# Optimization experiments

Measured on AMD Instinct MI355X. Metric: run time of the kernel, lower is better.

Reference implementation:

```python
import jax, jax.numpy as jnp
import numpy as np

NUM_CLASSES = 10
HIDDEN = 64
_LABEL2MASK_THRESHOL = 500


def setup_inputs() -> dict:
    key = jax.random.key(0)
    ks = jax.random.split(key, 8)
    B, h, w = 4, 60, 80
    feature1 = jax.random.normal(ks[0], (B, 512, h, w), dtype=jnp.float32)
    feature2 = jax.random.normal(ks[1], (B, 512, h // 2, w // 2), dtype=jnp.float32)
    # kaiming fan_in init for 1x1 convs: std = sqrt(2/fan_in)
    w1 = jax.random.normal(ks[2], (HIDDEN, 512), dtype=jnp.float32) * np.sqrt(2.0 / 512)
    b1 = jnp.zeros((HIDDEN,), dtype=jnp.float32)
    w2 = jax.random.normal(ks[3], (HIDDEN, 512), dtype=jnp.float32) * np.sqrt(2.0 / 512)
    b2 = jnp.zeros((HIDDEN,), dtype=jnp.float32)
    wo = jax.random.normal(ks[4], (NUM_CLASSES + 1, HIDDEN), dtype=jnp.float32) * np.sqrt(2.0 / HIDDEN)
    bo = jnp.zeros((NUM_CLASSES + 1,), dtype=jnp.float32)
    return {"feature1": feature1, "feature2": feature2, "w1": w1, "b1": b1,
            "w2": w2, "b2": b2, "wo": wo, "bo": bo}


def conv1x1(x, w, b):
    # x: (B,C,H,W), w: (O,C) -> (B,O,H,W)
    return jnp.einsum('bchw,oc->bohw', x, w) + b[None, :, None, None]


def label2bbx(seg, num_classes):
    # seg: (B,H,W) int labels. Vectorized per-(batch,class) min/max reduction
    # replacing the original python double loop. Fixed output shape
    # (B*(num_classes-1), 6); rows failing the pixel-count threshold are -1.
    B, H, W = seg.shape
    classes = jnp.arange(1, num_classes)  # cls_id != 0, covers 1..num_classes-1
    mask = seg[:, None, :, :] == classes[None, :, None, None]  # (B,C-1,H,W)
    count = mask.sum(axis=(2, 3))
    xs = jnp.arange(W)
    ys = jnp.arange(H)
    big = jnp.int32(2 ** 30)
    xmin = jnp.where(mask, xs[None, None, None, :], big).min(axis=(2, 3))
    xmax = jnp.where(mask, xs[None, None, None, :], -1).max(axis=(2, 3))
    ymin = jnp.where(mask, ys[None, None, :, None], big).min(axis=(2, 3))
    ymax = jnp.where(mask, ys[None, None, :, None], -1).max(axis=(2, 3))
    valid = count >= _LABEL2MASK_THRESHOL
    batch_ids = jnp.broadcast_to(jnp.arange(B)[:, None], (B, num_classes - 1))
    cls_ids = jnp.broadcast_to(classes[None, :], (B, num_classes - 1))
    rows = jnp.stack([batch_ids, xmin, ymin, xmax, ymax, cls_ids], axis=-1)
    rows = jnp.where(valid[..., None], rows, -1)
    return rows.reshape(-1, 6)


def reference(feature1, feature2, w1, b1, w2, b2, wo, bo):
    feat1 = jax.nn.relu(conv1x1(feature1, w1, b1))          # (B,64,h,w)
    feat2 = jax.nn.relu(conv1x1(feature2, w2, b2))          # (B,64,h/2,w/2)
    feat2_up = jnp.repeat(jnp.repeat(feat2, 2, axis=2), 2, axis=3)
    combo = feat1 + feat2_up
    # nearest upsample scale_factor=8
    combo_up = jnp.repeat(jnp.repeat(combo, 8, axis=2), 8, axis=3)  # (B,64,8h,8w)
    out = jax.nn.relu(conv1x1(combo_up, wo, bo))            # (B,11,8h,8w)
    probability = jax.nn.softmax(out, axis=1)
    segmentation = jnp.argmax(probability, axis=1)
    bbx = label2bbx(segmentation, NUM_CLASSES)
    return probability, segmentation, bbx
```

## Files before the change

kernel.cpp:

```cpp
#include <hip/hip_runtime.h>
#include <math.h>

#define NB   4
#define CIN  512
#define HID  64
#define NK   11
#define H1   60
#define W1p  80
#define P1   4800
#define H2   30
#define W2p  40
#define P2   1200
#define HO   480
#define WOp  640
#define NP1  (NB*P1)
#define NP2  (NB*P2)
#define PLANE ((size_t)HO*WOp)
#define SEG_OFF ((size_t)NB*NK*PLANE)
#define BBX_OFF (SEG_OFF + (size_t)NB*PLANE)

#define WS_C1  65536
#define WS_F2  (WS_C1 + NP1*64)
#define WS_PRB (WS_F2 + NP2*64)
#define WS_SEG (WS_PRB + NP1*12)

typedef __attribute__((ext_vector_type(8))) short bf16x8;
typedef __attribute__((ext_vector_type(4))) float f32x4;

__device__ __forceinline__ unsigned short bfsplit(float x, float& resid) {
    unsigned u = __float_as_uint(x);
    unsigned t = u + 0x7FFFu + ((u >> 16) & 1u);
    unsigned short h = (unsigned short)(t >> 16);
    resid = x - __uint_as_float((unsigned)h << 16);
    return h;
}

__global__ __launch_bounds__(256) void pack_w(const float* __restrict__ w1,
                                              const float* __restrict__ w2,
                                              float* __restrict__ ws) {
    int i = blockIdx.x * 256 + threadIdx.x;
    if (i >= HID * CIN) return;
    int o = i >> 9, c = i & 511;
    int chunk = c >> 6, r = c & 63, ks2 = r >> 5, k = r & 31;
    int lane = (o & 15) + ((k >> 3) << 4);
    int mt = o >> 4;
    int d = ((((chunk * 2 + ks2) * 4 + mt) * 2) * 64 + lane) * 8 + (k & 7);
    unsigned short* q = (unsigned short*)ws;
    float r1;
    unsigned short h = bfsplit(w1[i], r1);
    unsigned short m = bfsplit(r1, r1);
    q[d] = h; q[d + 512] = m;
    h = bfsplit(w2[i], r1); m = bfsplit(r1, r1);
    q[65536 + d] = h; q[65536 + d + 512] = m;
}

__global__ __launch_bounds__(256) void conv_mfma(const float* __restrict__ f1,
                                                 const float* __restrict__ f2,
                                                 const float* __restrict__ b1v,
                                                 const float* __restrict__ b2v,
                                                 const float* __restrict__ wsbase,
                                                 float* __restrict__ c1o,
                                                 float* __restrict__ f2o) {
    __shared__ int xpl[16 * 256];
    __shared__ int alds[16 * 256];
    int t = blockIdx.x;
    const float* X; const float* bias; float* Cout; const int* WPK;
    int P, px0;
    const unsigned short* q = (const unsigned short*)wsbase;
    if (t < 300) {
        int b = t / 75, ti = t % 75;
        px0 = ti * 64;
        X = f1 + (size_t)b * CIN * P1;  P = P1;  bias = b1v;
        WPK = (const int*)q;
        Cout = c1o + (size_t)b * P1 * 64;
    } else {
        int u = t - 300; int b = u / 19, ti = u % 19;
        px0 = ti * 64; if (px0 > P2 - 64) px0 = P2 - 64;
        X = f2 + (size_t)b * CIN * P2;  P = P2;  bias = b2v;
        WPK = (const int*)(q + 65536);
        Cout = f2o + (size_t)b * P2 * 64;
    }
    int tid  = threadIdx.x;
    int lane = tid & 63;
    int wv   = tid >> 6;
    int pcol = lane & 15, kgrp = lane >> 4;

    const float* Xg = X + px0 + wv * 16 + pcol;

    float xvA[16], xvB[16];
    int4 areg[4];

    auto loadX = [&](float* dst, int cc) {
#pragma unroll
        for (int ks2 = 0; ks2 < 2; ++ks2)
#pragma unroll
            for (int j = 0; j < 8; ++j) {
                int ch = cc * 64 + ks2 * 32 + kgrp * 8 + j;
                dst[ks2 * 8 + j] = Xg[(size_t)ch * P];
            }
    };
    auto loadA = [&](int cc) {
#pragma unroll
        for (int p = 0; p < 4; ++p)
            areg[p] = *(const int4*)&WPK[cc * 4096 + p * 1024 + tid * 4];
    };
    auto stage = [&](const float* xs) {
#pragma unroll
        for (int ks2 = 0; ks2 < 2; ++ks2) {
            int hh[8], mm[8];
#pragma unroll
            for (int j = 0; j < 8; ++j) {
                float r;
                unsigned short h = bfsplit(xs[ks2 * 8 + j], r);
                unsigned short m = bfsplit(r, r);
                hh[j] = h; mm[j] = m;
            }
            int4 H, M;
            ((int*)&H)[0] = hh[0] | (hh[1] << 16);
            ((int*)&H)[1] = hh[2] | (hh[3] << 16);
            ((int*)&H)[2] = hh[4] | (hh[5] << 16);
            ((int*)&H)[3] = hh[6] | (hh[7] << 16);
            ((int*)&M)[0] = mm[0] | (mm[1] << 16);
            ((int*)&M)[1] = mm[2] | (mm[3] << 16);
            ((int*)&M)[2] = mm[4] | (mm[5] << 16);
            ((int*)&M)[3] = mm[6] | (mm[7] << 16);
            int pg = ((wv * 2 + ks2) * 2) * 256 + lane * 4;
            *(int4*)&xpl[pg]       = H;
            *(int4*)&xpl[pg + 256] = M;
        }
#pragma unroll
        for (int p = 0; p < 4; ++p)
            *(int4*)&alds[p * 1024 + tid * 4] = areg[p];
    };

    union FU { int4 q; bf16x8 v; };
    f32x4 acc[4];
#pragma unroll
    for (int st = 0; st < 4; ++st) acc[st] = (f32x4){0.f, 0.f, 0.f, 0.f};

    loadX(xvA, 0);
    loadA(0);
    stage(xvA);
    loadX(xvA, 1);
    __syncthreads();

    for (int c = 0; c < 8; ++c) {
        if (c < 7) loadA(c + 1);
        if (c < 6) loadX(xvB, c + 2);
#pragma unroll
        for (int ks2 = 0; ks2 < 2; ++ks2) {
            FU Ah, Am;
            int pa = ((ks2 * 4 + wv) * 2) * 256 + lane * 4;
            Ah.q = *(const int4*)&alds[pa];
            Am.q = *(const int4*)&alds[pa + 256];
#pragma unroll
            for (int st = 0; st < 4; ++st) {
                FU Bh, Bm;
                int pb = ((st * 2 + ks2) * 2) * 256 + lane * 4;
                Bh.q = *(const int4*)&xpl[pb];
                Bm.q = *(const int4*)&xpl[pb + 256];
                acc[st] = __builtin_amdgcn_mfma_f32_16x16x32_bf16(Ah.v, Bh.v, acc[st], 0, 0, 0);
                acc[st] = __builtin_amdgcn_mfma_f32_16x16x32_bf16(Ah.v, Bm.v, acc[st], 0, 0, 0);
                acc[st] = __builtin_amdgcn_mfma_f32_16x16x32_bf16(Am.v, Bh.v, acc[st], 0, 0, 0);
                acc[st] = __builtin_amdgcn_mfma_f32_16x16x32_bf16(Am.v, Bm.v, acc[st], 0, 0, 0);
            }
        }
        __syncthreads();
        if (c < 7) {
            stage(xvA);
            __syncthreads();
#pragma unroll
            for (int i2 = 0; i2 < 16; ++i2) xvA[i2] = xvB[i2];
        }
    }

    int r4 = (lane >> 4) * 4;
    float4 bb = *(const float4*)(bias + wv * 16 + r4);
#pragma unroll
    for (int st = 0; st < 4; ++st) {
        int px = px0 + st * 16 + pcol;
        float a0 = acc[st][0] + bb.x;
        float a1 = acc[st][1] + bb.y;
        float a2 = acc[st][2] + bb.z;
        float a3 = acc[st][3] + bb.w;
        *(float4*)(Cout + (size_t)px * 64 + wv * 16 + r4) =
            make_float4(a0 > 0.f ? a0 : 0.f, a1 > 0.f ? a1 : 0.f,
                        a2 > 0.f ? a2 : 0.f, a3 > 0.f ? a3 : 0.f);
    }
}

__global__ __launch_bounds__(256) void head_kernel(const float* __restrict__ wo,
                                                   const float* __restrict__ bo,
                                                   float* __restrict__ ws) {
    __shared__ float swo[NK * 64];
    __shared__ float sbo[NK];
    for (int i = threadIdx.x; i < NK * 64; i += 256) swo[i] = wo[i];
    if (threadIdx.x < NK) sbo[threadIdx.x] = bo[threadIdx.x];
    __syncthreads();

    int p  = blockIdx.x * 256 + threadIdx.x;
    int b  = p / P1;
    int pb = p % P1;
    int y  = pb / W1p, x = pb % W1p;
    int qp = (y >> 1) * W2p + (x >> 1);
    const float* c1p = ws + WS_C1 + ((size_t)b * P1 + pb) * 64;
    const float* f2p = ws + WS_F2 + ((size_t)b * P2 + qp) * 64;

    float ok[NK];
#pragma unroll
    for (int k = 0; k < NK; ++k) ok[k] = sbo[k];
#pragma unroll
    for (int o4 = 0; o4 < 16; ++o4) {
        float4 c1q = *(const float4*)(c1p + o4 * 4);
        float4 f2q = *(const float4*)(f2p + o4 * 4);
        float co[4] = { c1q.x + f2q.x, c1q.y + f2q.y, c1q.z + f2q.z, c1q.w + f2q.w };
#pragma unroll
        for (int j = 0; j < 4; ++j) {
            int o = o4 * 4 + j;
#pragma unroll
            for (int k = 0; k < NK; ++k) ok[k] = fmaf(co[j], swo[k * 64 + o], ok[k]);
        }
    }
    float m = 0.f;
#pragma unroll
    for (int k = 0; k < NK; ++k) {
        ok[k] = ok[k] > 0.f ? ok[k] : 0.f;
        if (ok[k] > m) m = ok[k];
    }
    float e[NK], sum = 0.f;
#pragma unroll
    for (int k = 0; k < NK; ++k) { e[k] = expf(ok[k] - m); sum += e[k]; }
    float inv = 1.f / sum;
    int arg = 0; float best = ok[0];
#pragma unroll
    for (int k = 1; k < NK; ++k) { if (ok[k] > best) { best = ok[k]; arg = k; } }

    float* pr = ws + WS_PRB + (size_t)p * 12;
#pragma unroll
    for (int k = 0; k < NK; ++k) pr[k] = e[k] * inv;
    pr[11] = (float)arg;
    ((int*)(ws + WS_SEG))[p] = arg;
}

__global__ __launch_bounds__(256) void upsample_kernel(const float* __restrict__ ws,
                                                       float* __restrict__ out) {
    const float* prb = ws + WS_PRB;
    unsigned total4 = (unsigned)((SEG_OFF + (size_t)NB * PLANE) / 4);
    unsigned step = gridDim.x * 256;
    for (unsigned i4 = blockIdx.x * 256 + threadIdx.x; i4 < total4; i4 += step) {
        unsigned f = i4 * 4;
        float v;
        if (f < (unsigned)SEG_OFF) {
            unsigned plane = f / (unsigned)PLANE;
            unsigned r = f - plane * (unsigned)PLANE;
            unsigned b = plane / NK, k = plane - b * NK;
            unsigned y = r / WOp, x = r - y * WOp;
            unsigned p = b * P1 + (y >> 3) * W1p + (x >> 3);
            v = prb[p * 12 + k];
        } else {
            unsigned g = f - (unsigned)SEG_OFF;
            unsigned b = g / (unsigned)PLANE;
            unsigned r = g - b * (unsigned)PLANE;
            unsigned y = r / WOp, x = r - y * WOp;
            unsigned p = b * P1 + (y >> 3) * W1p + (x >> 3);
            v = prb[p * 12 + 11];
        }
        *(float4*)(out + f) = make_float4(v, v, v, v);
    }
}

__global__ __launch_bounds__(256) void bbx_kernel(const float* __restrict__ ws,
                                                  float* __restrict__ out) {
    __shared__ int cnt[10], xmn[10], xmx[10], ymn[10], ymx[10];
    int b = blockIdx.x;
    int t = threadIdx.x;
    if (t < 10) { cnt[t] = 0; xmn[t] = 1 << 30; xmx[t] = -1; ymn[t] = 1 << 30; ymx[t] = -1; }
    __syncthreads();
    const int* seg = (const int*)(ws + WS_SEG) + b * P1;
    for (int p = t; p < P1; p += 256) {
        int s = seg[p];
        if (s >= 1 && s <= 9) {
            int y = p / W1p, x = p % W1p;
            atomicAdd(&cnt[s], 1);
            atomicMin(&xmn[s], x); atomicMax(&xmx[s], x);
            atomicMin(&ymn[s], y); atomicMax(&ymx[s], y);
        }
    }
    __syncthreads();
    if (t < 9) {
        int c = t + 1;
        bool valid = cnt[c] * 64 >= 500;
        float r[6];
        if (valid) {
            r[0] = (float)b;
            r[1] = (float)(xmn[c] * 8);
            r[2] = (float)(ymn[c] * 8);
            r[3] = (float)(xmx[c] * 8 + 7);
            r[4] = (float)(ymx[c] * 8 + 7);
            r[5] = (float)c;
        } else {
            for (int i = 0; i < 6; ++i) r[i] = -1.f;
        }
        float* row = out + BBX_OFF + (size_t)(b * 9 + t) * 6;
        for (int i = 0; i < 6; ++i) row[i] = r[i];
    }
}

extern "C" void kernel_launch(void* const* d_in, const int* in_sizes, int n_in,
                              void* d_out, int out_size, void* d_ws, size_t ws_size,
                              hipStream_t stream) {
    const float* f1 = (const float*)d_in[0];
    const float* f2 = (const float*)d_in[1];
    const float* w1 = (const float*)d_in[2];
    const float* b1 = (const float*)d_in[3];
    const float* w2 = (const float*)d_in[4];
    const float* b2 = (const float*)d_in[5];
    const float* wo = (const float*)d_in[6];
    const float* bo = (const float*)d_in[7];
    float* ws  = (float*)d_ws;
    float* out = (float*)d_out;

    pack_w<<<128, 256, 0, stream>>>(w1, w2, ws);
    conv_mfma<<<376, 256, 0, stream>>>(f1, f2, b1, b2, ws,
                                       ws + WS_C1, ws + WS_F2);
    head_kernel<<<75, 256, 0, stream>>>(wo, bo, ws);
    upsample_kernel<<<2048, 256, 0, stream>>>(ws, out);
    bbx_kernel<<<NB, 256, 0, stream>>>(ws, out);
}
```

Baseline: 66.85 us.

## Double-buffer LDS tiles in conv MFMA loop to drop a barrier

Splits the shared-memory X and weight tiles into two buffers, so the next chunk can be staged into the idle buffer while the current one is read, removing one __syncthreads per iteration. Global prefetch distance drops from two chunks to one, which frees the extra register array, and a sched_barrier pins the load issue ahead of the MFMAs. The cost is double the LDS use, which may lower occupancy, and less latency hiding for the global loads.

Result: slower. 70.68 us (+5.7%).

```diff
diff --git a/kernel.cpp b/kernel.cpp
--- a/kernel.cpp
+++ b/kernel.cpp
@@ -61,8 +61,8 @@
                                                  const float* __restrict__ wsbase,
                                                  float* __restrict__ c1o,
                                                  float* __restrict__ f2o) {
-    __shared__ int xpl[16 * 256];
-    __shared__ int alds[16 * 256];
+    __shared__ int xpl[2][16 * 256];
+    __shared__ int alds[2][16 * 256];
     int t = blockIdx.x;
     const float* X; const float* bias; float* Cout; const int* WPK;
     int P, px0;
@@ -87,31 +87,31 @@
 
     const float* Xg = X + px0 + wv * 16 + pcol;
 
-    float xvA[16], xvB[16];
-    int4 areg[4];
-
-    auto loadX = [&](float* dst, int cc) {
+    float xvB[16];
+    int4 aregB[4];
+
+    auto loadX = [&](int cc) {
 #pragma unroll
         for (int ks2 = 0; ks2 < 2; ++ks2)
 #pragma unroll
             for (int j = 0; j < 8; ++j) {
                 int ch = cc * 64 + ks2 * 32 + kgrp * 8 + j;
-                dst[ks2 * 8 + j] = Xg[(size_t)ch * P];
+                xvB[ks2 * 8 + j] = Xg[(size_t)ch * P];
             }
     };
     auto loadA = [&](int cc) {
 #pragma unroll
         for (int p = 0; p < 4; ++p)
-            areg[p] = *(const int4*)&WPK[cc * 4096 + p * 1024 + tid * 4];
+            aregB[p] = *(const int4*)&WPK[cc * 4096 + p * 1024 + tid * 4];
     };
-    auto stage = [&](const float* xs) {
+    auto stage = [&](int buf) {
 #pragma unroll
         for (int ks2 = 0; ks2 < 2; ++ks2) {
             int hh[8], mm[8];
 #pragma unroll
             for (int j = 0; j < 8; ++j) {
                 float r;
-                unsigned short h = bfsplit(xs[ks2 * 8 + j], r);
+                unsigned short h = bfsplit(xvB[ks2 * 8 + j], r);
                 unsigned short m = bfsplit(r, r);
                 hh[j] = h; mm[j] = m;
             }
@@ -125,12 +125,12 @@
             ((int*)&M)[2] = mm[4] | (mm[5] << 16);
             ((int*)&M)[3] = mm[6] | (mm[7] << 16);
             int pg = ((wv * 2 + ks2) * 2) * 256 + lane * 4;
-            *(int4*)&xpl[pg]       = H;
-            *(int4*)&xpl[pg + 256] = M;
+            *(int4*)&xpl[buf][pg]       = H;
+            *(int4*)&xpl[buf][pg + 256] = M;
         }
 #pragma unroll
         for (int p = 0; p < 4; ++p)
-            *(int4*)&alds[p * 1024 + tid * 4] = areg[p];
+            *(int4*)&alds[buf][p * 1024 + tid * 4] = aregB[p];
     };
 
     union FU { int4 q; bf16x8 v; };
@@ -138,39 +138,39 @@
 #pragma unroll
     for (int st = 0; st < 4; ++st) acc[st] = (f32x4){0.f, 0.f, 0.f, 0.f};
 
-    loadX(xvA, 0);
-    loadA(0);
-    stage(xvA);
-    loadX(xvA, 1);
+    loadX(0); loadA(0);
+    stage(0);
     __syncthreads();
 
+    int cur = 0;
     for (int c = 0; c < 8; ++c) {
-        if (c < 7) loadA(c + 1);
-        if (c < 6) loadX(xvB, c + 2);
+        if (c < 7) {
+            loadX(c + 1);
+            loadA(c + 1);
+        }
+        __builtin_amdgcn_sched_barrier(0);
 #pragma unroll
         for (int ks2 = 0; ks2 < 2; ++ks2) {
             FU Ah, Am;
             int pa = ((ks2 * 4 + wv) * 2) * 256 + lane * 4;
-            Ah.q = *(const int4*)&alds[pa];
-            Am.q = *(const int4*)&alds[pa + 256];
+            Ah.q = *(const int4*)&alds[cur][pa];
+            Am.q = *(const int4*)&alds[cur][pa + 256];
 #pragma unroll
             for (int st = 0; st < 4; ++st) {
                 FU Bh, Bm;
                 int pb = ((st * 2 + ks2) * 2) * 256 + lane * 4;
-                Bh.q = *(const int4*)&xpl[pb];
-                Bm.q = *(const int4*)&xpl[pb + 256];
+                Bh.q = *(const int4*)&xpl[cur][pb];
+                Bm.q = *(const int4*)&xpl[cur][pb + 256];
                 acc[st] = __builtin_amdgcn_mfma_f32_16x16x32_bf16(Ah.v, Bh.v, acc[st], 0, 0, 0);
                 acc[st] = __builtin_amdgcn_mfma_f32_16x16x32_bf16(Ah.v, Bm.v, acc[st], 0, 0, 0);
                 acc[st] = __builtin_amdgcn_mfma_f32_16x16x32_bf16(Am.v, Bh.v, acc[st], 0, 0, 0);
                 acc[st] = __builtin_amdgcn_mfma_f32_16x16x32_bf16(Am.v, Bm.v, acc[st], 0, 0, 0);
             }
         }
-        __syncthreads();
         if (c < 7) {
-            stage(xvA);
+            stage(cur ^ 1);
             __syncthreads();
-#pragma unroll
-            for (int i2 = 0; i2 < 16; ++i2) xvA[i2] = xvB[i2];
+            cur ^= 1;
         }
     }
 
```

## Fuse feature1 conv, head, softmax and upsample into one kernel

Applied to the files above, without the earlier changes.

Splits the conv into a separate feature2 conv kernel and a fused kernel that runs the feature1 MFMA conv, keeps the 64-pixel tile result in shared memory, applies the head/softmax/argmax, and writes the upsampled probability and segmentation directly to the output. This removes the global round-trip of the feature1 conv output and the probability buffer, and drops two kernel launches. In exchange, the feature2 conv now runs serially before the fused kernel instead of alongside it. Only 64 threads do the head math, and the upsample writes are spread over just 300 blocks.

After: 80.93 us. 1.21x slower.

```diff
diff --git a/kernel.cpp b/kernel.cpp
--- a/kernel.cpp
+++ b/kernel.cpp
@@ -19,10 +19,8 @@
 #define SEG_OFF ((size_t)NB*NK*PLANE)
 #define BBX_OFF (SEG_OFF + (size_t)NB*PLANE)
 
-#define WS_C1  65536
-#define WS_F2  (WS_C1 + NP1*64)
-#define WS_PRB (WS_F2 + NP2*64)
-#define WS_SEG (WS_PRB + NP1*12)
+#define WS_F2  65536
+#define WS_SEG (WS_F2 + NP2*64)
 
 typedef __attribute__((ext_vector_type(8))) short bf16x8;
 typedef __attribute__((ext_vector_type(4))) float f32x4;
@@ -54,50 +52,33 @@
     q[65536 + d] = h; q[65536 + d + 512] = m;
 }
 
-__global__ __launch_bounds__(256) void conv_mfma(const float* __restrict__ f1,
-                                                 const float* __restrict__ f2,
-                                                 const float* __restrict__ b1v,
-                                                 const float* __restrict__ b2v,
-                                                 const float* __restrict__ wsbase,
-                                                 float* __restrict__ c1o,
-                                                 float* __restrict__ f2o) {
+__global__ __launch_bounds__(256) void conv_f2(const float* __restrict__ f2,
+                                               const float* __restrict__ b2v,
+                                               float* __restrict__ ws) {
     __shared__ int xpl[16 * 256];
     __shared__ int alds[16 * 256];
-    int t = blockIdx.x;
-    const float* X; const float* bias; float* Cout; const int* WPK;
-    int P, px0;
-    const unsigned short* q = (const unsigned short*)wsbase;
-    if (t < 300) {
-        int b = t / 75, ti = t % 75;
-        px0 = ti * 64;
-        X = f1 + (size_t)b * CIN * P1;  P = P1;  bias = b1v;
-        WPK = (const int*)q;
-        Cout = c1o + (size_t)b * P1 * 64;
-    } else {
-        int u = t - 300; int b = u / 19, ti = u % 19;
-        px0 = ti * 64; if (px0 > P2 - 64) px0 = P2 - 64;
-        X = f2 + (size_t)b * CIN * P2;  P = P2;  bias = b2v;
-        WPK = (const int*)(q + 65536);
-        Cout = f2o + (size_t)b * P2 * 64;
-    }
+    int u = blockIdx.x;
+    int b = u / 19, ti = u % 19;
+    int px0 = ti * 64; if (px0 > P2 - 64) px0 = P2 - 64;
+    const float* X = f2 + (size_t)b * CIN * P2;
+    const int P = P2;
+    const int* WPK = (const int*)((const unsigned short*)ws + 65536);
+    float* Cout = ws + WS_F2 + (size_t)b * P2 * 64;
+
     int tid  = threadIdx.x;
     int lane = tid & 63;
     int wv   = tid >> 6;
     int pcol = lane & 15, kgrp = lane >> 4;
-
     const float* Xg = X + px0 + wv * 16 + pcol;
 
     float xvA[16], xvB[16];
     int4 areg[4];
-
     auto loadX = [&](float* dst, int cc) {
 #pragma unroll
         for (int ks2 = 0; ks2 < 2; ++ks2)
 #pragma unroll
-            for (int j = 0; j < 8; ++j) {
-                int ch = cc * 64 + ks2 * 32 + kgrp * 8 + j;
-                dst[ks2 * 8 + j] = Xg[(size_t)ch * P];
-            }
+            for (int j = 0; j < 8; ++j)
+                dst[ks2 * 8 + j] = Xg[(size_t)(cc * 64 + ks2 * 32 + kgrp * 8 + j) * P];
     };
     auto loadA = [&](int cc) {
 #pragma unroll
@@ -116,14 +97,10 @@
                 hh[j] = h; mm[j] = m;
             }
             int4 H, M;
-            ((int*)&H)[0] = hh[0] | (hh[1] << 16);
-            ((int*)&H)[1] = hh[2] | (hh[3] << 16);
-            ((int*)&H)[2] = hh[4] | (hh[5] << 16);
-            ((int*)&H)[3] = hh[6] | (hh[7] << 16);
-            ((int*)&M)[0] = mm[0] | (mm[1] << 16);
-            ((int*)&M)[1] = mm[2] | (mm[3] << 16);
-            ((int*)&M)[2] = mm[4] | (mm[5] << 16);
-            ((int*)&M)[3] = mm[6] | (mm[7] << 16);
+            ((int*)&H)[0] = hh[0] | (hh[1] << 16); ((int*)&H)[1] = hh[2] | (hh[3] << 16);
+            ((int*)&H)[2] = hh[4] | (hh[5] << 16); ((int*)&H)[3] = hh[6] | (hh[7] << 16);
+            ((int*)&M)[0] = mm[0] | (mm[1] << 16); ((int*)&M)[1] = mm[2] | (mm[3] << 16);
+            ((int*)&M)[2] = mm[4] | (mm[5] << 16); ((int*)&M)[3] = mm[6] | (mm[7] << 16);
             int pg = ((wv * 2 + ks2) * 2) * 256 + lane * 4;
             *(int4*)&xpl[pg]       = H;
             *(int4*)&xpl[pg + 256] = M;
@@ -138,12 +115,8 @@
 #pragma unroll
     for (int st = 0; st < 4; ++st) acc[st] = (f32x4){0.f, 0.f, 0.f, 0.f};
 
-    loadX(xvA, 0);
-    loadA(0);
-    stage(xvA);
-    loadX(xvA, 1);
-    __syncthreads();
-
+    loadX(xvA, 0); loadA(0); stage(xvA); loadX(xvA, 1);
+    __syncthreads();
     for (int c = 0; c < 8; ++c) {
         if (c < 7) loadA(c + 1);
         if (c < 6) loadX(xvB, c + 2);
@@ -173,99 +146,194 @@
             for (int i2 = 0; i2 < 16; ++i2) xvA[i2] = xvB[i2];
         }
     }
-
     int r4 = (lane >> 4) * 4;
-    float4 bb = *(const float4*)(bias + wv * 16 + r4);
+    float4 bb = *(const float4*)(b2v + wv * 16 + r4);
 #pragma unroll
     for (int st = 0; st < 4; ++st) {
         int px = px0 + st * 16 + pcol;
-        float a0 = acc[st][0] + bb.x;
-        float a1 = acc[st][1] + bb.y;
-        float a2 = acc[st][2] + bb.z;
-        float a3 = acc[st][3] + bb.w;
+        float a0 = acc[st][0] + bb.x, a1 = acc[st][1] + bb.y;
+        float a2 = acc[st][2] + bb.z, a3 = acc[st][3] + bb.w;
         *(float4*)(Cout + (size_t)px * 64 + wv * 16 + r4) =
             make_float4(a0 > 0.f ? a0 : 0.f, a1 > 0.f ? a1 : 0.f,
                         a2 > 0.f ? a2 : 0.f, a3 > 0.f ? a3 : 0.f);
     }
 }
 
-__global__ __launch_bounds__(256) void head_kernel(const float* __restrict__ wo,
+__global__ __launch_bounds__(256) void mega_kernel(const float* __restrict__ f1,
+                                                   const float* __restrict__ b1v,
+                                                   const float* __restrict__ wo,
                                                    const float* __restrict__ bo,
-                                                   float* __restrict__ ws) {
-    __shared__ float swo[NK * 64];
-    __shared__ float sbo[NK];
-    for (int i = threadIdx.x; i < NK * 64; i += 256) swo[i] = wo[i];
-    if (threadIdx.x < NK) sbo[threadIdx.x] = bo[threadIdx.x];
-    __syncthreads();
-
-    int p  = blockIdx.x * 256 + threadIdx.x;
-    int b  = p / P1;
-    int pb = p % P1;
-    int y  = pb / W1p, x = pb % W1p;
-    int qp = (y >> 1) * W2p + (x >> 1);
-    const float* c1p = ws + WS_C1 + ((size_t)b * P1 + pb) * 64;
-    const float* f2p = ws + WS_F2 + ((size_t)b * P2 + qp) * 64;
-
-    float ok[NK];
-#pragma unroll
-    for (int k = 0; k < NK; ++k) ok[k] = sbo[k];
-#pragma unroll
-    for (int o4 = 0; o4 < 16; ++o4) {
-        float4 c1q = *(const float4*)(c1p + o4 * 4);
-        float4 f2q = *(const float4*)(f2p + o4 * 4);
-        float co[4] = { c1q.x + f2q.x, c1q.y + f2q.y, c1q.z + f2q.z, c1q.w + f2q.w };
-#pragma unroll
-        for (int j = 0; j < 4; ++j) {
-            int o = o4 * 4 + j;
-#pragma unroll
-            for (int k = 0; k < NK; ++k) ok[k] = fmaf(co[j], swo[k * 64 + o], ok[k]);
-        }
-    }
-    float m = 0.f;
-#pragma unroll
-    for (int k = 0; k < NK; ++k) {
-        ok[k] = ok[k] > 0.f ? ok[k] : 0.f;
-        if (ok[k] > m) m = ok[k];
-    }
-    float e[NK], sum = 0.f;
-#pragma unroll
-    for (int k = 0; k < NK; ++k) { e[k] = expf(ok[k] - m); sum += e[k]; }
-    float inv = 1.f / sum;
-    int arg = 0; float best = ok[0];
-#pragma unroll
-    for (int k = 1; k < NK; ++k) { if (ok[k] > best) { best = ok[k]; arg = k; } }
-
-    float* pr = ws + WS_PRB + (size_t)p * 12;
-#pragma unroll
-    for (int k = 0; k < NK; ++k) pr[k] = e[k] * inv;
-    pr[11] = (float)arg;
-    ((int*)(ws + WS_SEG))[p] = arg;
-}
-
-__global__ __launch_bounds__(256) void upsample_kernel(const float* __restrict__ ws,
-                                                       float* __restrict__ out) {
-    const float* prb = ws + WS_PRB;
-    unsigned total4 = (unsigned)((SEG_OFF + (size_t)NB * PLANE) / 4);
-    unsigned step = gridDim.x * 256;
-    for (unsigned i4 = blockIdx.x * 256 + threadIdx.x; i4 < total4; i4 += step) {
-        unsigned f = i4 * 4;
-        float v;
-        if (f < (unsigned)SEG_OFF) {
-            unsigned plane = f / (unsigned)PLANE;
-            unsigned r = f - plane * (unsigned)PLANE;
-            unsigned b = plane / NK, k = plane - b * NK;
-            unsigned y = r / WOp, x = r - y * WOp;
-            unsigned p = b * P1 + (y >> 3) * W1p + (x >> 3);
-            v = prb[p * 12 + k];
-        } else {
-            unsigned g = f - (unsigned)SEG_OFF;
-            unsigned b = g / (unsigned)PLANE;
-            unsigned r = g - b * (unsigned)PLANE;
-            unsigned y = r / WOp, x = r - y * WOp;
-            unsigned p = b * P1 + (y >> 3) * W1p + (x >> 3);
-            v = prb[p * 12 + 11];
-        }
-        *(float4*)(out + f) = make_float4(v, v, v, v);
+                                                   float* __restrict__ ws,
+                                                   float* __restrict__ out) {
+    __shared__ int smem[8192];
+    int* xpl  = smem;
+    int* alds = smem + 4096;
+    int t = blockIdx.x;
+    int b = t / 75, ti = t % 75;
+    int px0 = ti * 64;
+    const float* X = f1 + (size_t)b * CIN * P1;
+    const int P = P1;
+    const int* WPK = (const int*)ws;
+
+    int tid  = threadIdx.x;
+    int lane = tid & 63;
+    int wv   = tid >> 6;
+    int pcol = lane & 15, kgrp = lane >> 4;
+    const float* Xg = X + px0 + wv * 16 + pcol;
+
+    float xvA[16], xvB[16];
+    int4 areg[4];
+    auto loadX = [&](float* dst, int cc) {
+#pragma unroll
+        for (int ks2 = 0; ks2 < 2; ++ks2)
+#pragma unroll
+            for (int j = 0; j < 8; ++j)
+                dst[ks2 * 8 + j] = Xg[(size_t)(cc * 64 + ks2 * 32 + kgrp * 8 + j) * P];
+    };
+    auto loadA = [&](int cc) {
+#pragma unroll
+        for (int p = 0; p < 4; ++p)
+            areg[p] = *(const int4*)&WPK[cc * 4096 + p * 1024 + tid * 4];
+    };
+    auto stage = [&](const float* xs) {
+#pragma unroll
+        for (int ks2 = 0; ks2 < 2; ++ks2) {
+            int hh[8], mm[8];
+#pragma unroll
+            for (int j = 0; j < 8; ++j) {
+                float r;
+                unsigned short h = bfsplit(xs[ks2 * 8 + j], r);
+                unsigned short m = bfsplit(r, r);
+                hh[j] = h; mm[j] = m;
+            }
+            int4 H, M;
+            ((int*)&H)[0] = hh[0] | (hh[1] << 16); ((int*)&H)[1] = hh[2] | (hh[3] << 16);
+            ((int*)&H)[2] = hh[4] | (hh[5] << 16); ((int*)&H)[3] = hh[6] | (hh[7] << 16);
+            ((int*)&M)[0] = mm[0] | (mm[1] << 16); ((int*)&M)[1] = mm[2] | (mm[3] << 16);
+            ((int*)&M)[2] = mm[4] | (mm[5] << 16); ((int*)&M)[3] = mm[6] | (mm[7] << 16);
+            int pg = ((wv * 2 + ks2) * 2) * 256 + lane * 4;
+            *(int4*)&xpl[pg]       = H;
+            *(int4*)&xpl[pg + 256] = M;
+        }
+#pragma unroll
+        for (int p = 0; p < 4; ++p)
+            *(int4*)&alds[p * 1024 + tid * 4] = areg[p];
+    };
+
+    union FU { int4 q; bf16x8 v; };
+    f32x4 acc[4];
+#pragma unroll
+    for (int st = 0; st < 4; ++st) acc[st] = (f32x4){0.f, 0.f, 0.f, 0.f};
+
+    loadX(xvA, 0); loadA(0); stage(xvA); loadX(xvA, 1);
+    __syncthreads();
+    for (int c = 0; c < 8; ++c) {
+        if (c < 7) loadA(c + 1);
+        if (c < 6) loadX(xvB, c + 2);
+#pragma unroll
+        for (int ks2 = 0; ks2 < 2; ++ks2) {
+            FU Ah, Am;
+            int pa = ((ks2 * 4 + wv) * 2) * 256 + lane * 4;
+            Ah.q = *(const int4*)&alds[pa];
+            Am.q = *(const int4*)&alds[pa + 256];
+#pragma unroll
+            for (int st = 0; st < 4; ++st) {
+                FU Bh, Bm;
+                int pb = ((st * 2 + ks2) * 2) * 256 + lane * 4;
+                Bh.q = *(const int4*)&xpl[pb];
+                Bm.q = *(const int4*)&xpl[pb + 256];
+                acc[st] = __builtin_amdgcn_mfma_f32_16x16x32_bf16(Ah.v, Bh.v, acc[st], 0, 0, 0);
+                acc[st] = __builtin_amdgcn_mfma_f32_16x16x32_bf16(Ah.v, Bm.v, acc[st], 0, 0, 0);
+                acc[st] = __builtin_amdgcn_mfma_f32_16x16x32_bf16(Am.v, Bh.v, acc[st], 0, 0, 0);
+                acc[st] = __builtin_amdgcn_mfma_f32_16x16x32_bf16(Am.v, Bm.v, acc[st], 0, 0, 0);
+            }
+        }
+        __syncthreads();
+        if (c < 7) {
+            stage(xvA);
+            __syncthreads();
+#pragma unroll
+            for (int i2 = 0; i2 < 16; ++i2) xvA[i2] = xvB[i2];
+        }
+    }
+    __syncthreads();
+
+    float* c1   = (float*)smem;
+    float* prob = c1 + 4352;
+    float* swo  = prob + 832;
+    float* sbo  = swo + 704;
+
+    int r4 = (lane >> 4) * 4;
+    float4 bb = *(const float4*)(b1v + wv * 16 + r4);
+#pragma unroll
+    for (int st = 0; st < 4; ++st) {
+        float a0 = acc[st][0] + bb.x, a1 = acc[st][1] + bb.y;
+        float a2 = acc[st][2] + bb.z, a3 = acc[st][3] + bb.w;
+        *(float4*)&c1[(st * 16 + pcol) * 68 + wv * 16 + r4] =
+            make_float4(a0 > 0.f ? a0 : 0.f, a1 > 0.f ? a1 : 0.f,
+                        a2 > 0.f ? a2 : 0.f, a3 > 0.f ? a3 : 0.f);
+    }
+    for (int i = tid; i < NK * 64; i += 256) swo[i] = wo[i];
+    if (tid < NK) sbo[tid] = bo[tid];
+    __syncthreads();
+
+    if (tid < 64) {
+        int px_g = px0 + tid;
+        int y = px_g / W1p, x = px_g % W1p;
+        int qp = (y >> 1) * W2p + (x >> 1);
+        const float* f2p = ws + WS_F2 + ((size_t)b * P2 + qp) * 64;
+        const float* c1p = c1 + tid * 68;
+        float ok[NK];
+#pragma unroll
+        for (int k = 0; k < NK; ++k) ok[k] = sbo[k];
+#pragma unroll
+        for (int o4 = 0; o4 < 16; ++o4) {
+            float4 cq = *(const float4*)(c1p + o4 * 4);
+            float4 fq = *(const float4*)(f2p + o4 * 4);
+            float co[4] = { cq.x + fq.x, cq.y + fq.y, cq.z + fq.z, cq.w + fq.w };
+#pragma unroll
+            for (int j = 0; j < 4; ++j) {
+                int o = o4 * 4 + j;
+#pragma unroll
+                for (int k = 0; k < NK; ++k) ok[k] = fmaf(co[j], swo[k * 64 + o], ok[k]);
+            }
+        }
+        float m = 0.f;
+#pragma unroll
+        for (int k = 0; k < NK; ++k) {
+            ok[k] = ok[k] > 0.f ? ok[k] : 0.f;
+            if (ok[k] > m) m = ok[k];
+        }
+        float e[NK], sum = 0.f;
+#pragma unroll
+        for (int k = 0; k < NK; ++k) { e[k] = expf(ok[k] - m); sum += e[k]; }
+        float inv = 1.f / sum;
+        int arg = 0; float best = ok[0];
+#pragma unroll
+        for (int k = 1; k < NK; ++k) { if (ok[k] > best) { best = ok[k]; arg = k; } }
+#pragma unroll
+        for (int k = 0; k < NK; ++k) prob[tid * 13 + k] = e[k] * inv;
+        prob[tid * 13 + 11] = (float)arg;
+        ((int*)(ws + WS_SEG))[b * P1 + px_g] = arg;
+    }
+    __syncthreads();
+
+    for (int id = tid; id < 12 * 8 * 128; id += 256) {
+        int k   = id >> 10;
+        int rem = id & 1023;
+        int dy  = rem >> 7;
+        int g   = rem & 127;
+        int j   = g >> 1;
+        int q   = g & 1;
+        int px_g = px0 + j;
+        int y = px_g / W1p, x = px_g % W1p;
+        float v = prob[j * 13 + k];
+        size_t base;
+        if (k < NK)
+            base = (((size_t)(b * NK + k) * HO) + (size_t)(y * 8 + dy)) * WOp + x * 8 + q * 4;
+        else
+            base = SEG_OFF + (((size_t)b * HO) + (size_t)(y * 8 + dy)) * WOp + x * 8 + q * 4;
+        *(float4*)(out + base) = make_float4(v, v, v, v);
     }
 }
 
@@ -321,9 +389,7 @@
     float* out = (float*)d_out;
 
     pack_w<<<128, 256, 0, stream>>>(w1, w2, ws);
-    conv_mfma<<<376, 256, 0, stream>>>(f1, f2, b1, b2, ws,
-                                       ws + WS_C1, ws + WS_F2);
-    head_kernel<<<75, 256, 0, stream>>>(wo, bo, ws);
-    upsample_kernel<<<2048, 256, 0, stream>>>(ws, out);
+    conv_f2<<<76, 256, 0, stream>>>(f2, b2, ws);
+    mega_kernel<<<300, 256, 0, stream>>>(f1, b1, wo, bo, ws, out);
     bbx_kernel<<<NB, 256, 0, stream>>>(ws, out);
 }
```

## Shrink conv pixel tile to 16 per block and launch 1500 blocks

Applied to the files above, without the earlier changes.

Each conv block now covers 16 pixels instead of 64, which raises the grid from 376 to 1500 blocks to fill more compute units. The LDS staging layout for activations is reworked so all 256 threads cooperatively load and split 4 channels each. The cost is that the weight tile is reloaded into LDS four times as often overall, and each block does less MFMA work between barriers. Strided activation loads now cover only 16 contiguous floats per channel row.

Measured after the change: 98.43 us. 47.2% more time.

```diff
diff --git a/kernel.cpp b/kernel.cpp
--- a/kernel.cpp
+++ b/kernel.cpp
@@ -5,10 +5,10 @@
 #define CIN  512
 #define HID  64
 #define NK   11
-#define H1   60
+#define HH1  60
 #define W1p  80
 #define P1   4800
-#define H2   30
+#define HH2  30
 #define W2p  40
 #define P2   1200
 #define HO   480
@@ -61,21 +61,21 @@
                                                  const float* __restrict__ wsbase,
                                                  float* __restrict__ c1o,
                                                  float* __restrict__ f2o) {
-    __shared__ int xpl[16 * 256];
+    __shared__ int xpl[1024];
     __shared__ int alds[16 * 256];
     int t = blockIdx.x;
     const float* X; const float* bias; float* Cout; const int* WPK;
     int P, px0;
     const unsigned short* q = (const unsigned short*)wsbase;
-    if (t < 300) {
-        int b = t / 75, ti = t % 75;
-        px0 = ti * 64;
+    if (t < 1200) {
+        int b = t / 300, ti = t % 300;
+        px0 = ti * 16;
         X = f1 + (size_t)b * CIN * P1;  P = P1;  bias = b1v;
         WPK = (const int*)q;
         Cout = c1o + (size_t)b * P1 * 64;
     } else {
-        int u = t - 300; int b = u / 19, ti = u % 19;
-        px0 = ti * 64; if (px0 > P2 - 64) px0 = P2 - 64;
+        int u = t - 1200; int b = u / 75, ti = u % 75;
+        px0 = ti * 16;
         X = f2 + (size_t)b * CIN * P2;  P = P2;  bias = b2v;
         WPK = (const int*)(q + 65536);
         Cout = f2o + (size_t)b * P2 * 64;
@@ -83,21 +83,22 @@
     int tid  = threadIdx.x;
     int lane = tid & 63;
     int wv   = tid >> 6;
-    int pcol = lane & 15, kgrp = lane >> 4;
-
-    const float* Xg = X + px0 + wv * 16 + pcol;
-
-    float xvA[16], xvB[16];
+    int pcol = lane & 15;
+    int px_s = tid & 15;
+    int cg   = tid >> 4;
+    int s_ks2 = cg >> 3;
+    int s_lane = px_s + ((cg & 7) >> 1) * 16;
+    int s_w0   = (cg & 1) * 2;
+
+    const float* Xg = X + px0 + px_s;
+
+    float xvA[4], xvB[4];
     int4 areg[4];
 
     auto loadX = [&](float* dst, int cc) {
 #pragma unroll
-        for (int ks2 = 0; ks2 < 2; ++ks2)
-#pragma unroll
-            for (int j = 0; j < 8; ++j) {
-                int ch = cc * 64 + ks2 * 32 + kgrp * 8 + j;
-                dst[ks2 * 8 + j] = Xg[(size_t)ch * P];
-            }
+        for (int j = 0; j < 4; ++j)
+            dst[j] = Xg[(size_t)(cc * 64 + cg * 4 + j) * P];
     };
     auto loadA = [&](int cc) {
 #pragma unroll
@@ -105,88 +106,65 @@
             areg[p] = *(const int4*)&WPK[cc * 4096 + p * 1024 + tid * 4];
     };
     auto stage = [&](const float* xs) {
-#pragma unroll
-        for (int ks2 = 0; ks2 < 2; ++ks2) {
-            int hh[8], mm[8];
-#pragma unroll
-            for (int j = 0; j < 8; ++j) {
-                float r;
-                unsigned short h = bfsplit(xs[ks2 * 8 + j], r);
-                unsigned short m = bfsplit(r, r);
-                hh[j] = h; mm[j] = m;
-            }
-            int4 H, M;
-            ((int*)&H)[0] = hh[0] | (hh[1] << 16);
-            ((int*)&H)[1] = hh[2] | (hh[3] << 16);
-            ((int*)&H)[2] = hh[4] | (hh[5] << 16);
-            ((int*)&H)[3] = hh[6] | (hh[7] << 16);
-            ((int*)&M)[0] = mm[0] | (mm[1] << 16);
-            ((int*)&M)[1] = mm[2] | (mm[3] << 16);
-            ((int*)&M)[2] = mm[4] | (mm[5] << 16);
-            ((int*)&M)[3] = mm[6] | (mm[7] << 16);
-            int pg = ((wv * 2 + ks2) * 2) * 256 + lane * 4;
-            *(int4*)&xpl[pg]       = H;
-            *(int4*)&xpl[pg + 256] = M;
-        }
+        unsigned short h[4], m[4];
+#pragma unroll
+        for (int j = 0; j < 4; ++j) {
+            float r;
+            h[j] = bfsplit(xs[j], r);
+            m[j] = bfsplit(r, r);
+        }
+        int vH0 = (int)h[0] | ((int)h[1] << 16);
+        int vH1 = (int)h[2] | ((int)h[3] << 16);
+        int vM0 = (int)m[0] | ((int)m[1] << 16);
+        int vM1 = (int)m[2] | ((int)m[3] << 16);
+        int bh = ((s_ks2 * 2 + 0) * 64 + s_lane) * 4 + s_w0;
+        int bm = ((s_ks2 * 2 + 1) * 64 + s_lane) * 4 + s_w0;
+        xpl[bh] = vH0; xpl[bh + 1] = vH1;
+        xpl[bm] = vM0; xpl[bm + 1] = vM1;
 #pragma unroll
         for (int p = 0; p < 4; ++p)
             *(int4*)&alds[p * 1024 + tid * 4] = areg[p];
     };
 
     union FU { int4 q; bf16x8 v; };
-    f32x4 acc[4];
-#pragma unroll
-    for (int st = 0; st < 4; ++st) acc[st] = (f32x4){0.f, 0.f, 0.f, 0.f};
-
-    loadX(xvA, 0);
-    loadA(0);
-    stage(xvA);
-    loadX(xvA, 1);
+    f32x4 acc = (f32x4){0.f, 0.f, 0.f, 0.f};
+
+    loadX(xvA, 0); loadA(0); stage(xvA); loadX(xvA, 1);
     __syncthreads();
-
     for (int c = 0; c < 8; ++c) {
         if (c < 7) loadA(c + 1);
         if (c < 6) loadX(xvB, c + 2);
 #pragma unroll
         for (int ks2 = 0; ks2 < 2; ++ks2) {
-            FU Ah, Am;
+            FU Ah, Am, Bh, Bm;
             int pa = ((ks2 * 4 + wv) * 2) * 256 + lane * 4;
             Ah.q = *(const int4*)&alds[pa];
             Am.q = *(const int4*)&alds[pa + 256];
-#pragma unroll
-            for (int st = 0; st < 4; ++st) {
-                FU Bh, Bm;
-                int pb = ((st * 2 + ks2) * 2) * 256 + lane * 4;
-                Bh.q = *(const int4*)&xpl[pb];
-                Bm.q = *(const int4*)&xpl[pb + 256];
-                acc[st] = __builtin_amdgcn_mfma_f32_16x16x32_bf16(Ah.v, Bh.v, acc[st], 0, 0, 0);
-                acc[st] = __builtin_amdgcn_mfma_f32_16x16x32_bf16(Ah.v, Bm.v, acc[st], 0, 0, 0);
-                acc[st] = __builtin_amdgcn_mfma_f32_16x16x32_bf16(Am.v, Bh.v, acc[st], 0, 0, 0);
-                acc[st] = __builtin_amdgcn_mfma_f32_16x16x32_bf16(Am.v, Bm.v, acc[st], 0, 0, 0);
-            }
+            int pb = (ks2 * 2) * 256 + lane * 4;
+            Bh.q = *(const int4*)&xpl[pb];
+            Bm.q = *(const int4*)&xpl[pb + 256];
+            acc = __builtin_amdgcn_mfma_f32_16x16x32_bf16(Ah.v, Bh.v, acc, 0, 0, 0);
+            acc = __builtin_amdgcn_mfma_f32_16x16x32_bf16(Ah.v, Bm.v, acc, 0, 0, 0);
+            acc = __builtin_amdgcn_mfma_f32_16x16x32_bf16(Am.v, Bh.v, acc, 0, 0, 0);
+            acc = __builtin_amdgcn_mfma_f32_16x16x32_bf16(Am.v, Bm.v, acc, 0, 0, 0);
         }
         __syncthreads();
         if (c < 7) {
             stage(xvA);
             __syncthreads();
 #pragma unroll
-            for (int i2 = 0; i2 < 16; ++i2) xvA[i2] = xvB[i2];
+            for (int i2 = 0; i2 < 4; ++i2) xvA[i2] = xvB[i2];
         }
     }
 
     int r4 = (lane >> 4) * 4;
     float4 bb = *(const float4*)(bias + wv * 16 + r4);
-#pragma unroll
-    for (int st = 0; st < 4; ++st) {
-        int px = px0 + st * 16 + pcol;
-        float a0 = acc[st][0] + bb.x;
-        float a1 = acc[st][1] + bb.y;
-        float a2 = acc[st][2] + bb.z;
-        float a3 = acc[st][3] + bb.w;
-        *(float4*)(Cout + (size_t)px * 64 + wv * 16 + r4) =
-            make_float4(a0 > 0.f ? a0 : 0.f, a1 > 0.f ? a1 : 0.f,
-                        a2 > 0.f ? a2 : 0.f, a3 > 0.f ? a3 : 0.f);
-    }
+    int px = px0 + pcol;
+    float a0 = acc[0] + bb.x, a1 = acc[1] + bb.y;
+    float a2 = acc[2] + bb.z, a3 = acc[3] + bb.w;
+    *(float4*)(Cout + (size_t)px * 64 + wv * 16 + r4) =
+        make_float4(a0 > 0.f ? a0 : 0.f, a1 > 0.f ? a1 : 0.f,
+                    a2 > 0.f ? a2 : 0.f, a3 > 0.f ? a3 : 0.f);
 }
 
 __global__ __launch_bounds__(256) void head_kernel(const float* __restrict__ wo,
@@ -321,8 +299,8 @@
     float* out = (float*)d_out;
 
     pack_w<<<128, 256, 0, stream>>>(w1, w2, ws);
-    conv_mfma<<<376, 256, 0, stream>>>(f1, f2, b1, b2, ws,
-                                       ws + WS_C1, ws + WS_F2);
+    conv_mfma<<<1500, 256, 0, stream>>>(f1, f2, b1, b2, ws,
+                                        ws + WS_C1, ws + WS_F2);
     head_kernel<<<75, 256, 0, stream>>>(wo, bo, ws);
     upsample_kernel<<<2048, 256, 0, stream>>>(ws, out);
     bbx_kernel<<<NB, 256, 0, stream>>>(ws, out);
```
